# Kernel tuning notes

Hardware: AMD Instinct MI355X
Metric: run time of the kernel (lower is better)

The kernel has to match this reference:

```python
import jax, jax.numpy as jnp
import numpy as np

N_NODES = 100000   # graph size N
DIM     = 128      # embedding dim d
M_SEL   = 4096     # selected nodes per forward
N_POS   = 32       # positives per node (padded/fixed sample of pos_neigh)
N_NEG   = 256      # negatives per node (fixed sample of neg_samples)


def setup_inputs() -> dict:
    key = jax.random.key(0)
    ks = jax.random.split(key, 8)
    return {
        "P": jax.random.normal(ks[0], (N_NODES, DIM), dtype=jnp.float32),
        "W_d": jax.random.normal(ks[1], (DIM,), dtype=jnp.float32),
        "deg_vec": jax.random.uniform(ks[2], (N_NODES,), dtype=jnp.float32) * 64.0,
        "nodes": jax.random.randint(ks[3], (M_SEL,), 0, N_NODES),
        "pos_idx": jax.random.randint(ks[4], (M_SEL, N_POS), 0, N_NODES),
        "neg_idx": jax.random.randint(ks[5], (M_SEL, N_NEG), 0, N_NODES),
        "deg_pos_idx": jax.random.randint(ks[6], (M_SEL, N_POS), 0, N_NODES),
        "deg_neg_idx": jax.random.randint(ks[7], (M_SEL, N_NEG), 0, N_NODES),
    }


def my_sigmoid(x):
    # Sigmoid_alt: sign-carrying sigmoid in (-1, 1) (parity used in the repo's plots)
    return 2.0 * jax.nn.sigmoid(x) - 1.0


def _contrast(Z, nodes, pos_idx, neg_idx):
    # softmax_formula vectorized over the selected-node batch:
    #   loss_i = -( mean_p hamming(Z_i, Z_p) - log sum_n exp(hamming(Z_i, Z_n)) )
    Zi = Z[nodes]                                            # [M, d]
    h_pos = jnp.abs(Zi[:, None, :] - Z[pos_idx]).sum(-1)    # [M, P]
    h_neg = jnp.abs(Zi[:, None, :] - Z[neg_idx]).sum(-1)    # [M, K]
    log_sum_neg = jax.scipy.special.logsumexp(h_neg, axis=1)  # stable log(sum(exp(.)))
    per_node = log_sum_neg - h_pos.mean(axis=1)
    return per_node.sum()


def reference(P, W_d, deg_vec, nodes, pos_idx, neg_idx, deg_pos_idx, deg_neg_idx):
    Z = my_sigmoid(P)                                        # [N, d]
    # degree_loss: MSE(Z @ W_d, deg_vec)
    L_deg = jnp.mean((Z @ W_d - deg_vec) ** 2)
    # contrast_adj_n_degDist: adjacency and degree-distribution contrastive totals
    L_adj = _contrast(Z, nodes, pos_idx, neg_idx)
    L_deg_dist = _contrast(Z, nodes, deg_pos_idx, deg_neg_idx)
    return (L_adj, L_deg_dist, L_deg)
```

## Files before the change

kernel.cpp:

```cpp
#include <hip/hip_runtime.h>
#include <math.h>

#define N_NODES_C 100000
#define DIM_C     128
#define M_SEL_C   4096
#define N_POS_C   32
#define N_NEG_C   256
#define QS4       (2.0f / 15.0f)

__device__ __forceinline__ float wsum64(float v) {
#pragma unroll
    for (int o = 32; o; o >>= 1) v += __shfl_xor(v, o, 64);
    return v;
}
__device__ __forceinline__ float hsum32(float v) {
#pragma unroll
    for (int o = 1; o < 32; o <<= 1) v += __shfl_xor(v, o, 64);
    return v;
}
__device__ __forceinline__ int gsum4(int v) {
    v += __shfl_xor(v, 1, 64);
    v += __shfl_xor(v, 2, 64);
    return v;
}

__device__ __forceinline__ unsigned sad8(unsigned a, unsigned b, unsigned acc) {
    unsigned d;
    asm volatile("v_sad_u8 %0, %1, %2, %3" : "=v"(d) : "v"(a), "v"(b), "v"(acc));
    return d;
}

__device__ __forceinline__ int sadrow4(uint4 b, const unsigned* cl, const unsigned* ch) {
    const unsigned M = 0x0F0F0F0Fu;
    unsigned s = 0;
    s = sad8(b.x & M, cl[0], s); s = sad8((b.x >> 4) & M, ch[0], s);
    s = sad8(b.y & M, cl[1], s); s = sad8((b.y >> 4) & M, ch[1], s);
    s = sad8(b.z & M, cl[2], s); s = sad8((b.z >> 4) & M, ch[2], s);
    s = sad8(b.w & M, cl[3], s); s = sad8((b.w >> 4) & M, ch[3], s);
    return (int)s;
}

__global__ __launch_bounds__(256) void k_z_deg(
    const float* __restrict__ P, const float* __restrict__ Wd,
    const float* __restrict__ deg, unsigned short* __restrict__ Qh,
    float* __restrict__ out)
{
    const int lane = threadIdx.x & 63;
    const int sl   = lane & 31;
    const int hi   = lane >> 5;
    const int wv   = threadIdx.x >> 6;
    const int gw   = blockIdx.x * 4 + wv;
    const int nw   = gridDim.x * 4;
    const float4 w = *(const float4*)(Wd + 4 * sl);
    float acc = 0.0f;
    for (int pr = gw; pr < N_NODES_C / 2; pr += nw) {
        const int row = 2 * pr + hi;
        float4 p = *(const float4*)(P + (size_t)row * DIM_C + 4 * sl);
        float r0 = __fdividef(15.0f, 1.0f + __expf(-p.x));
        float r1 = __fdividef(15.0f, 1.0f + __expf(-p.y));
        float r2 = __fdividef(15.0f, 1.0f + __expf(-p.z));
        float r3 = __fdividef(15.0f, 1.0f + __expf(-p.w));
        unsigned q = __float2uint_rn(r0) | (__float2uint_rn(r1) << 4) |
                     (__float2uint_rn(r2) << 8) | (__float2uint_rn(r3) << 12);
        Qh[(size_t)row * (DIM_C / 4) + sl] = (unsigned short)q;
        float z0 = fmaf(r0, QS4, -1.0f), z1 = fmaf(r1, QS4, -1.0f);
        float z2 = fmaf(r2, QS4, -1.0f), z3 = fmaf(r3, QS4, -1.0f);
        float d4 = fmaf(z0, w.x, fmaf(z1, w.y, fmaf(z2, w.z, z3 * w.w)));
        d4 = hsum32(d4);
        if (sl == 0) { float d = d4 - deg[row]; acc = fmaf(d, d, acc); }
    }
    __shared__ float part[4];
    float a = wsum64(acc);
    if (lane == 0) part[wv] = a;
    __syncthreads();
    if (threadIdx.x == 0)
        atomicAdd(out + 2, (part[0] + part[1] + part[2] + part[3]) * (1.0f / N_NODES_C));
}

__global__ __launch_bounds__(256, 8) void k_contrast(
    const uint4* __restrict__ Q4,
    const int* __restrict__ nodes,
    const int* __restrict__ pos_a, const int* __restrict__ neg_a,
    const int* __restrict__ pos_b, const int* __restrict__ neg_b,
    float* __restrict__ out)
{
    const int tid  = threadIdx.x;
    const int wv   = tid >> 6;
    const int lane = tid & 63;
    const int l4   = lane & 3;
    const int g    = lane >> 2;

    const int id   = blockIdx.x * 4 + wv;
    const int pr   = id >> 1;
    const int half = id & 1;
    const int sel  = pr >> 12;
    const int m    = pr & (M_SEL_C - 1);
    const int* __restrict__ pos_idx = sel ? pos_b : pos_a;
    const int* __restrict__ neg_idx = sel ? neg_b : neg_a;

    const int node = nodes[m];
    uint4 c = Q4[((unsigned)node << 2) + l4];
    const unsigned M = 0x0F0F0F0Fu;
    unsigned cl[4] = { c.x & M, c.y & M, c.z & M, c.w & M };
    unsigned ch[4] = { (c.x >> 4) & M, (c.y >> 4) & M, (c.z >> 4) & M, (c.w >> 4) & M };

    const int* __restrict__ np = neg_idx + m * N_NEG_C + half * 128;
    int nn[8];
#pragma unroll
    for (int t = 0; t < 8; ++t) nn[t] = np[t * 16 + g];

    uint4 nb[4];
#pragma unroll
    for (int u = 0; u < 4; ++u) nb[u] = Q4[((unsigned)nn[u] << 2) + l4];

    float mx = -1e30f, sm = 0.0f;
#pragma unroll
    for (int t = 0; t < 8; ++t) {
        int s = gsum4(sadrow4(nb[t & 3], cl, ch));
        if (t < 4) nb[t & 3] = Q4[((unsigned)nn[t + 4] << 2) + l4];
        float v = (float)s * QS4;
        float nm = fmaxf(mx, v);
        sm = fmaf(sm, __expf(mx - nm), __expf(v - nm));
        mx = nm;
    }

    float ps = 0.0f;
    if (half) {
        const int* __restrict__ pq = pos_idx + m * N_POS_C;
        int p0 = pq[g], p1 = pq[16 + g];
        uint4 b0 = Q4[((unsigned)p0 << 2) + l4];
        uint4 b1 = Q4[((unsigned)p1 << 2) + l4];
        ps = (float)(sadrow4(b0, cl, ch) + sadrow4(b1, cl, ch));
    }

#pragma unroll
    for (int o = 1; o < 4; o <<= 1) ps += __shfl_xor(ps, o, 64);
#pragma unroll
    for (int o = 4; o < 64; o <<= 1) {
        float om = __shfl_xor(mx, o, 64);
        float os = __shfl_xor(sm, o, 64);
        float nm = fmaxf(mx, om);
        sm = fmaf(sm, __expf(mx - nm), os * __expf(om - nm));
        mx = nm;
        ps += __shfl_xor(ps, o, 64);
    }

    __shared__ float mrgM[4], mrgS[4], mrgP[4];
    if (lane == 0) { mrgM[wv] = mx; mrgS[wv] = sm; mrgP[wv] = ps; }
    __syncthreads();
    if (!(wv & 1) && lane == 0) {
        float m0 = mrgM[wv],     s0 = mrgS[wv];
        float m1 = mrgM[wv + 1], s1 = mrgS[wv + 1];
        float nm = fmaxf(m0, m1);
        float st = fmaf(s0, __expf(m0 - nm), s1 * __expf(m1 - nm));
        float lse = nm + __logf(st);
        float pm  = (mrgP[wv] + mrgP[wv + 1]) * QS4 * (1.0f / N_POS_C);
        atomicAdd(out + sel, lse - pm);
    }
}

extern "C" void kernel_launch(void* const* d_in, const int* in_sizes, int n_in,
                              void* d_out, int out_size, void* d_ws, size_t ws_size,
                              hipStream_t stream) {
    const float* P    = (const float*)d_in[0];
    const float* Wd   = (const float*)d_in[1];
    const float* deg  = (const float*)d_in[2];
    const int* nodes  = (const int*)d_in[3];
    const int* pos_i  = (const int*)d_in[4];
    const int* neg_i  = (const int*)d_in[5];
    const int* dpos_i = (const int*)d_in[6];
    const int* dneg_i = (const int*)d_in[7];
    float* out = (float*)d_out;
    unsigned short* Qh = (unsigned short*)d_ws;

    hipMemsetAsync(out, 0, (size_t)out_size * sizeof(float), stream);
    k_z_deg<<<2048, 256, 0, stream>>>(P, Wd, deg, Qh, out);
    k_contrast<<<4096, 256, 0, stream>>>(
        (const uint4*)Qh, nodes, pos_i, neg_i, dpos_i, dneg_i, out);
}
```

Measured before the change: 237.8 us.

## Bin contrast pairs by target row block to reuse shared-memory slices

Measured after the change: 411.0 us. 72.8% more time.

```diff
diff --git a/kernel.cpp b/kernel.cpp
--- a/kernel.cpp
+++ b/kernel.cpp
@@ -8,6 +8,21 @@
 #define N_NEG_C   256
 #define QS4       (2.0f / 15.0f)
 
+#define RPB    256
+#define BINS   391
+#define CELLS  (BINS * 2)
+#define ABLK   64
+#define CAP    104
+#define SV_CAP 6144
+
+#define OFF_QH     0u
+#define OFF_CNT    6400256u
+#define OFF_BUCKET 6600448u
+#define OFF_SVALS  27420416u
+#define OFF_PART   37029632u
+#define OFF_PS     49841920u
+#define WS_NEED    49874688u
+
 __device__ __forceinline__ float wsum64(float v) {
 #pragma unroll
     for (int o = 32; o; o >>= 1) v += __shfl_xor(v, o, 64);
@@ -23,13 +38,16 @@
     v += __shfl_xor(v, 2, 64);
     return v;
 }
-
 __device__ __forceinline__ unsigned sad8(unsigned a, unsigned b, unsigned acc) {
     unsigned d;
     asm volatile("v_sad_u8 %0, %1, %2, %3" : "=v"(d) : "v"(a), "v"(b), "v"(acc));
     return d;
 }
-
+__device__ __forceinline__ unsigned nib(unsigned a, unsigned b, unsigned acc) {
+    const unsigned M = 0x0F0F0F0Fu;
+    acc = sad8(a & M, b & M, acc);
+    return sad8((a >> 4) & M, (b >> 4) & M, acc);
+}
 __device__ __forceinline__ int sadrow4(uint4 b, const unsigned* cl, const unsigned* ch) {
     const unsigned M = 0x0F0F0F0Fu;
     unsigned s = 0;
@@ -77,6 +95,150 @@
         atomicAdd(out + 2, (part[0] + part[1] + part[2] + part[3]) * (1.0f / N_NODES_C));
 }
 
+__global__ __launch_bounds__(1024) void k_binA(
+    const int* __restrict__ pos_a, const int* __restrict__ neg_a,
+    const int* __restrict__ pos_b, const int* __restrict__ neg_b,
+    unsigned* __restrict__ bucket, unsigned* __restrict__ cnt)
+{
+    __shared__ unsigned lcnt[CELLS];
+    const int tid = threadIdx.x;
+    const int blk = blockIdx.x;
+    for (int i = tid; i < CELLS; i += 1024) lcnt[i] = 0u;
+    __syncthreads();
+
+    auto put = [&](int r, int pair, int slot) {
+        int bin  = r >> 8;
+        int rl   = r & 255;
+        int cell = (bin << 1) | (pair >> 12);
+        unsigned pos = atomicAdd(&lcnt[cell], 1u);
+        if (pos < CAP)
+            bucket[(size_t)(cell * ABLK + blk) * CAP + pos] =
+                ((unsigned)rl << 22) | ((unsigned)pair << 9) | (unsigned)slot;
+    };
+
+    for (int i = blk * 1024 + tid; i < M_SEL_C * N_POS_C; i += ABLK * 1024)
+        put(pos_a[i], i >> 5, i & 31);
+    for (int i = blk * 1024 + tid; i < M_SEL_C * N_NEG_C; i += ABLK * 1024)
+        put(neg_a[i], i >> 8, 32 + (i & 255));
+    for (int i = blk * 1024 + tid; i < M_SEL_C * N_POS_C; i += ABLK * 1024)
+        put(pos_b[i], 4096 + (i >> 5), i & 31);
+    for (int i = blk * 1024 + tid; i < M_SEL_C * N_NEG_C; i += ABLK * 1024)
+        put(neg_b[i], 4096 + (i >> 8), 32 + (i & 255));
+
+    __syncthreads();
+    for (int c = tid; c < CELLS; c += 1024)
+        cnt[c * ABLK + blk] = min(lcnt[c], (unsigned)CAP);
+}
+
+__global__ __launch_bounds__(256) void k_binB(
+    const unsigned* __restrict__ QhU32, const int* __restrict__ nodes,
+    const unsigned* __restrict__ bucket, const unsigned* __restrict__ cnt,
+    unsigned short* __restrict__ svals, unsigned* __restrict__ part,
+    int* __restrict__ Ps)
+{
+    __shared__ unsigned slice[RPB * 16];
+    __shared__ int      hmaxS[4096];
+    __shared__ float    Sacc[4096];
+    __shared__ unsigned pref[ABLK + 1];
+    __shared__ unsigned carr[ABLK];
+
+    const int tid  = threadIdx.x;
+    const int cell = blockIdx.x;
+    const int bin  = cell >> 1;
+    const int rbase = bin * RPB;
+    const int nr    = min(RPB, N_NODES_C - rbase);
+
+    for (int k = tid; k < nr * 16; k += 256) slice[k] = QhU32[(size_t)rbase * 16 + k];
+    for (int k = tid; k < 4096; k += 256) { hmaxS[k] = -1; Sacc[k] = 0.0f; }
+    if (tid < ABLK) carr[tid] = cnt[cell * ABLK + tid];
+    __syncthreads();
+    if (tid == 0) {
+        unsigned run = 0;
+        for (int j = 0; j < ABLK; ++j) { pref[j] = run; run += carr[j]; }
+        pref[ABLK] = run;
+    }
+    __syncthreads();
+    const unsigned T = min(pref[ABLK], (unsigned)SV_CAP);
+
+    for (unsigned i = tid; i < T; i += 256) {
+        int lo = 0, hi = ABLK;
+        while (hi - lo > 1) { int md = (lo + hi) >> 1; if (pref[md] <= i) lo = md; else hi = md; }
+        unsigned e = bucket[(size_t)(cell * ABLK + lo) * CAP + (i - pref[lo])];
+        int slot = e & 511;
+        int pair = (e >> 9) & 8191;
+        int rl   = (e >> 22) & 255;
+        int m    = pair & 4095;
+        int node = nodes[m];
+        const uint4* c4 = (const uint4*)(QhU32 + (size_t)node * 16);
+        const uint4* b4 = (const uint4*)(slice + rl * 16);
+        unsigned s = 0;
+#pragma unroll
+        for (int k = 0; k < 4; ++k) {
+            uint4 a = c4[k];
+            uint4 b = b4[k];
+            s = nib(a.x, b.x, s); s = nib(a.y, b.y, s);
+            s = nib(a.z, b.z, s); s = nib(a.w, b.w, s);
+        }
+        svals[(size_t)cell * SV_CAP + i] = (unsigned short)s;
+        if (slot < 32) atomicAdd(&Ps[pair], (int)s);
+        else           atomicMax(&hmaxS[m], (int)s);
+    }
+    __syncthreads();
+
+    for (unsigned i = tid; i < T; i += 256) {
+        int lo = 0, hi = ABLK;
+        while (hi - lo > 1) { int md = (lo + hi) >> 1; if (pref[md] <= i) lo = md; else hi = md; }
+        unsigned e = bucket[(size_t)(cell * ABLK + lo) * CAP + (i - pref[lo])];
+        int slot = e & 511;
+        if (slot >= 32) {
+            int m = (e >> 9) & 4095;
+            int s = (int)svals[(size_t)cell * SV_CAP + i];
+            unsafeAtomicAdd(&Sacc[m], __expf((float)(s - hmaxS[m]) * QS4));
+        }
+    }
+    __syncthreads();
+
+    for (int m2 = tid; m2 < 4096; m2 += 256) {
+        int hm = hmaxS[m2];
+        unsigned pv;
+        if (hm < 0) pv = 0xFFFFu;
+        else {
+            unsigned su = __float_as_uint(Sacc[m2]) + 0x8000u;
+            pv = (unsigned)hm | (su & 0xFFFF0000u);
+        }
+        part[(size_t)cell * 4096 + m2] = pv;
+    }
+}
+
+__global__ __launch_bounds__(256) void k_binC(
+    const unsigned* __restrict__ part, const int* __restrict__ Ps,
+    float* __restrict__ out)
+{
+    const int tid  = threadIdx.x;
+    const int pair = blockIdx.x * 256 + tid;
+    const int sel  = pair >> 12;
+    const int m    = pair & 4095;
+
+    float M = -1.0f, S = 0.0f;
+    for (int b = 0; b < BINS; ++b) {
+        unsigned pv = part[(size_t)((b << 1) | sel) * 4096 + m];
+        unsigned hm = pv & 0xFFFFu;
+        if (hm == 0xFFFFu) continue;
+        float Mc = (float)hm;
+        float Sc = __uint_as_float(pv & 0xFFFF0000u);
+        if (Mc > M) { S = fmaf(S, __expf((M - Mc) * QS4), Sc); M = Mc; }
+        else        { S = fmaf(Sc, __expf((Mc - M) * QS4), S); }
+    }
+    float lse = M * QS4 + __logf(S);
+    float val = lse - (float)Ps[pair] * QS4 * (1.0f / N_POS_C);
+
+    __shared__ float red[4];
+    float v = wsum64(val);
+    if ((tid & 63) == 0) red[tid >> 6] = v;
+    __syncthreads();
+    if (tid == 0) atomicAdd(out + sel, red[0] + red[1] + red[2] + red[3]);
+}
+
 __global__ __launch_bounds__(256, 8) void k_contrast(
     const uint4* __restrict__ Q4,
     const int* __restrict__ nodes,
@@ -108,7 +270,6 @@
     int nn[8];
 #pragma unroll
     for (int t = 0; t < 8; ++t) nn[t] = np[t * 16 + g];
-
     uint4 nb[4];
 #pragma unroll
     for (int u = 0; u < 4; ++u) nb[u] = Q4[((unsigned)nn[u] << 2) + l4];
@@ -171,10 +332,26 @@
     const int* dpos_i = (const int*)d_in[6];
     const int* dneg_i = (const int*)d_in[7];
     float* out = (float*)d_out;
-    unsigned short* Qh = (unsigned short*)d_ws;
+    char* w = (char*)d_ws;
+    unsigned short* Qh = (unsigned short*)(w + OFF_QH);
 
     hipMemsetAsync(out, 0, (size_t)out_size * sizeof(float), stream);
     k_z_deg<<<2048, 256, 0, stream>>>(P, Wd, deg, Qh, out);
-    k_contrast<<<4096, 256, 0, stream>>>(
-        (const uint4*)Qh, nodes, pos_i, neg_i, dpos_i, dneg_i, out);
-}
+
+    if (ws_size >= WS_NEED) {
+        unsigned* cnt    = (unsigned*)(w + OFF_CNT);
+        unsigned* bucket = (unsigned*)(w + OFF_BUCKET);
+        unsigned short* sv = (unsigned short*)(w + OFF_SVALS);
+        unsigned* part   = (unsigned*)(w + OFF_PART);
+        int* Ps          = (int*)(w + OFF_PS);
+
+        hipMemsetAsync(Ps, 0, 8192 * sizeof(int), stream);
+        k_binA<<<ABLK, 1024, 0, stream>>>(pos_i, neg_i, dpos_i, dneg_i, bucket, cnt);
+        k_binB<<<CELLS, 256, 0, stream>>>((const unsigned*)Qh, nodes, bucket, cnt,
+                                          sv, part, Ps);
+        k_binC<<<32, 256, 0, stream>>>(part, Ps, out);
+    } else {
+        k_contrast<<<4096, 256, 0, stream>>>(
+            (const uint4*)Qh, nodes, pos_i, neg_i, dpos_i, dneg_i, out);
+    }
+}
```
